# Kernel optimization log

Measured on AMD Instinct MI355X. Metric: run time of the kernel, lower is better.

The kernel has to match this reference:

```python
import jax, jax.numpy as jnp
import numpy as np
import math

B, T, D, H = 2, 2048, 1024, 16
DH = D // H  # 64


def _rope_tables(seq_len, dim, dtype=jnp.float32):
    inv_freq = 1.0 / (10000.0 ** (jnp.arange(0, dim, 2, dtype=jnp.float32) / dim))
    t = jnp.arange(seq_len, dtype=jnp.float32)
    freqs = jnp.outer(t, inv_freq)  # [T, dim/2]
    return jnp.cos(freqs).astype(dtype), jnp.sin(freqs).astype(dtype)


def apply_rotary(x, cos, sin):
    # x: [B,H,T,DH]; cos/sin: [1,1,T,DH/2]
    d = x.shape[-1]
    x1, x2 = x[..., : d // 2], x[..., d // 2 :]
    return jnp.concatenate([x1 * cos - x2 * sin, x2 * cos + x1 * sin], axis=-1)


def setup_inputs() -> dict:
    key = jax.random.key(0)
    k1, k2, k3 = jax.random.split(key, 3)
    x = jax.random.normal(k1, (B, T, D), dtype=jnp.float32)
    Wqkv = jax.random.normal(k2, (D, 3 * D), dtype=jnp.float32) * (1.0 / math.sqrt(D))
    Wout = jax.random.normal(k3, (D, D), dtype=jnp.float32) * (1.0 / math.sqrt(D))
    cos, sin = _rope_tables(T, DH)  # [T, 32]
    mask = jnp.tril(jnp.ones((T, T), dtype=bool))[None, None]  # causal [1,1,T,T]
    return {"x": x, "Wqkv": Wqkv, "Wout": Wout, "cos": cos, "sin": sin, "mask": mask}


def reference(x, Wqkv, Wout, cos, sin, mask):
    Bb, Tt, C = x.shape
    qkv = (x @ Wqkv).reshape(Bb, Tt, 3, H, DH)
    q = jnp.transpose(qkv[:, :, 0], (0, 2, 1, 3))  # [B,H,T,DH]
    k = jnp.transpose(qkv[:, :, 1], (0, 2, 1, 3))
    v = jnp.transpose(qkv[:, :, 2], (0, 2, 1, 3))
    c = cos[None, None]  # [1,1,T,DH/2]
    s = sin[None, None]
    q = apply_rotary(q, c, s)
    k = apply_rotary(k, c, s)
    attn = jnp.einsum("bhqd,bhkd->bhqk", q, k) / math.sqrt(DH)
    attn = jnp.where(mask, attn, jnp.float32(-jnp.inf))
    attn = jax.nn.softmax(attn, axis=-1)  # dropout p=0 (eval)
    out = jnp.einsum("bhqk,bhkd->bhqd", attn, v)
    out = jnp.transpose(out, (0, 2, 1, 3)).reshape(Bb, Tt, C)
    return out @ Wout
```

## Files before the change

### kernel.cpp

```cpp
#include <hip/hip_runtime.h>
#include <hip/hip_bf16.h>

#define B_ 2
#define T_ 2048
#define D_ 1024
#define H_ 16
#define DH_ 64
#define N3_ 3072
#define M_ 4096

typedef __attribute__((ext_vector_type(8))) short short8;
typedef __attribute__((ext_vector_type(4))) float f32x4;
typedef __attribute__((ext_vector_type(4))) unsigned short ushort4v;

__device__ __forceinline__ unsigned short f2bf(float f) {
  return __builtin_bit_cast(unsigned short, __hip_bfloat16(f));
}
__device__ __forceinline__ float bf2f(unsigned short u) {
  union { unsigned u; float f; } v; v.u = ((unsigned)u) << 16;
  return v.f;
}

__device__ __forceinline__ void gload_lds16(const unsigned short* g, unsigned short* l) {
  __builtin_amdgcn_global_load_lds((const __attribute__((address_space(1))) void*)g,
                                   (__attribute__((address_space(3))) void*)l, 16, 0, 0);
}

__global__ __launch_bounds__(256)
void k_cvt(const float* __restrict__ in, unsigned short* __restrict__ out) {
  int i = (blockIdx.x * 256 + threadIdx.x) * 4;
  f32x4 v = *(const f32x4*)&in[i];
  ushort4v o;
  o[0] = f2bf(v[0]); o[1] = f2bf(v[1]); o[2] = f2bf(v[2]); o[3] = f2bf(v[3]);
  *(ushort4v*)&out[i] = o;
}

__global__ __launch_bounds__(256)
void k_transpose(const float* __restrict__ in, unsigned short* __restrict__ out,
                 int R, int C) {
  __shared__ float tile[64][65];
  int c0 = blockIdx.x * 64, r0 = blockIdx.y * 64;
  int tx = threadIdx.x & 63, ty = threadIdx.x >> 6;
#pragma unroll
  for (int i = 0; i < 64; i += 4)
    tile[ty + i][tx] = in[(size_t)(r0 + ty + i) * C + c0 + tx];
  __syncthreads();
#pragma unroll
  for (int i = 0; i < 64; i += 4)
    out[(size_t)(c0 + ty + i) * R + r0 + tx] = f2bf(tile[tx][ty + i]);
}

template <typename OUT_T>
__global__ __launch_bounds__(256)
void k_gemm_bt(const unsigned short* __restrict__ A, const unsigned short* __restrict__ Bt,
               OUT_T* __restrict__ C, int Mx, int Nx, int Kx) {
  __shared__ __align__(16) unsigned short As[128 * 64];
  __shared__ __align__(16) unsigned short Bs[128 * 64];
  const int tid = threadIdx.x;
  const int lane = tid & 63;
  const int l15 = lane & 15, lg = lane >> 4;
  const int l8 = lane >> 3, c8 = lane & 7;
  const int wid = tid >> 6;
  const int wr = wid >> 1, wc = wid & 1;
  const int m0 = blockIdx.y * 128, n0 = blockIdx.x * 128;

  const f32x4 zero4 = {0.f, 0.f, 0.f, 0.f};
  f32x4 acc[4][4];
#pragma unroll
  for (int mi = 0; mi < 4; ++mi)
#pragma unroll
    for (int ni = 0; ni < 4; ++ni) acc[mi][ni] = zero4;

  for (int k0 = 0; k0 < Kx; k0 += 64) {
#pragma unroll
    for (int i = 0; i < 4; ++i)
      gload_lds16(&A[(size_t)(m0 + wid * 32 + i * 8 + l8) * Kx + k0 + c8 * 8],
                  &As[(wid * 32 + i * 8) * 64]);
#pragma unroll
    for (int i = 0; i < 4; ++i)
      gload_lds16(&Bt[(size_t)(n0 + wid * 32 + i * 8 + l8) * Kx + k0 + c8 * 8],
                  &Bs[(wid * 32 + i * 8) * 64]);
    __syncthreads();
#pragma unroll
    for (int kk = 0; kk < 2; ++kk) {
      short8 af[4], bfr[4];
#pragma unroll
      for (int mi = 0; mi < 4; ++mi)
        af[mi] = *(const short8*)&As[(wr * 64 + mi * 16 + l15) * 64 + kk * 32 + lg * 8];
#pragma unroll
      for (int ni = 0; ni < 4; ++ni)
        bfr[ni] = *(const short8*)&Bs[(wc * 64 + ni * 16 + l15) * 64 + kk * 32 + lg * 8];
#pragma unroll
      for (int mi = 0; mi < 4; ++mi)
#pragma unroll
        for (int ni = 0; ni < 4; ++ni)
          acc[mi][ni] = __builtin_amdgcn_mfma_f32_16x16x32_bf16(af[mi], bfr[ni], acc[mi][ni], 0, 0, 0);
    }
    __syncthreads();
  }
#pragma unroll
  for (int mi = 0; mi < 4; ++mi)
#pragma unroll
    for (int ni = 0; ni < 4; ++ni)
#pragma unroll
      for (int j = 0; j < 4; ++j) {
        int row = m0 + wr * 64 + mi * 16 + lg * 4 + j;
        int col = n0 + wc * 64 + ni * 16 + l15;
        float v = acc[mi][ni][j];
        if constexpr (sizeof(OUT_T) == 2) C[(size_t)row * Nx + col] = f2bf(v);
        else                              C[(size_t)row * Nx + col] = v;
      }
}

__global__ __launch_bounds__(256)
void k_gemm_qkv_rope(const unsigned short* __restrict__ A, const unsigned short* __restrict__ Bt,
                     const float* __restrict__ cosT, const float* __restrict__ sinT,
                     unsigned short* __restrict__ Q, unsigned short* __restrict__ K,
                     unsigned short* __restrict__ Vt) {
  __shared__ __align__(16) unsigned short As[128 * 64];
  __shared__ __align__(16) unsigned short Bs[128 * 64];
  const int Kx = D_, Nx = N3_;
  const int tid = threadIdx.x;
  const int lane = tid & 63;
  const int l15 = lane & 15, lg = lane >> 4;
  const int l8 = lane >> 3, c8 = lane & 7;
  const int wid = tid >> 6;
  const int wr = wid >> 1, wc = wid & 1;
  const int m0 = blockIdx.y * 128, n0 = blockIdx.x * 128;

  const f32x4 zero4 = {0.f, 0.f, 0.f, 0.f};
  f32x4 acc[4][4];
#pragma unroll
  for (int mi = 0; mi < 4; ++mi)
#pragma unroll
    for (int ni = 0; ni < 4; ++ni) acc[mi][ni] = zero4;

  for (int k0 = 0; k0 < Kx; k0 += 64) {
#pragma unroll
    for (int i = 0; i < 4; ++i)
      gload_lds16(&A[(size_t)(m0 + wid * 32 + i * 8 + l8) * Kx + k0 + c8 * 8],
                  &As[(wid * 32 + i * 8) * 64]);
#pragma unroll
    for (int i = 0; i < 4; ++i)
      gload_lds16(&Bt[(size_t)(n0 + wid * 32 + i * 8 + l8) * Kx + k0 + c8 * 8],
                  &Bs[(wid * 32 + i * 8) * 64]);
    __syncthreads();
#pragma unroll
    for (int kk = 0; kk < 2; ++kk) {
      short8 af[4], bfr[4];
#pragma unroll
      for (int mi = 0; mi < 4; ++mi)
        af[mi] = *(const short8*)&As[(wr * 64 + mi * 16 + l15) * 64 + kk * 32 + lg * 8];
#pragma unroll
      for (int ni = 0; ni < 4; ++ni)
        bfr[ni] = *(const short8*)&Bs[(wc * 64 + ni * 16 + l15) * 64 + kk * 32 + lg * 8];
#pragma unroll
      for (int mi = 0; mi < 4; ++mi)
#pragma unroll
        for (int ni = 0; ni < 4; ++ni)
          acc[mi][ni] = __builtin_amdgcn_mfma_f32_16x16x32_bf16(af[mi], bfr[ni], acc[mi][ni], 0, 0, 0);
    }
    __syncthreads();
  }

  const int region = n0 >> 10;
  const int h = (((n0 & 1023)) + wc * 64) >> 6;
  if (region < 2) {
    unsigned short* out = (region == 0) ? Q : K;
    const float scale = (region == 0) ? 0.125f : 1.f;
#pragma unroll
    for (int mi = 0; mi < 4; ++mi)
#pragma unroll
      for (int j = 0; j < 4; ++j) {
        int row = m0 + wr * 64 + mi * 16 + lg * 4 + j;
        int b = row >> 11, t = row & (T_ - 1);
        size_t obase = ((size_t)(b * H_ + h) * T_ + t) * DH_;
#pragma unroll
        for (int ni = 0; ni < 2; ++ni) {
          int dh = ni * 16 + l15;
          float cs = cosT[t * 32 + dh], sn = sinT[t * 32 + dh];
          float x1 = acc[mi][ni][j], x2 = acc[mi][ni + 2][j];
          out[obase + dh]      = f2bf((x1 * cs - x2 * sn) * scale);
          out[obase + dh + 32] = f2bf((x2 * cs + x1 * sn) * scale);
        }
      }
  } else {
#pragma unroll
    for (int mi = 0; mi < 4; ++mi) {
      int row0 = m0 + wr * 64 + mi * 16 + lg * 4;
      int b = row0 >> 11, t0 = row0 & (T_ - 1);
#pragma unroll
      for (int ni = 0; ni < 4; ++ni) {
        int col = (n0 - 2048) + wc * 64 + ni * 16 + l15;
        int hv = col >> 6, dh = col & 63;
        ushort4v pk;
#pragma unroll
        for (int j = 0; j < 4; ++j) pk[j] = f2bf(acc[mi][ni][j]);
        *(ushort4v*)&Vt[((size_t)(b * H_ + hv) * DH_ + dh) * T_ + t0] = pk;
      }
    }
  }
}

__global__ __launch_bounds__(256)
void k_attn(const unsigned short* __restrict__ Q, const unsigned short* __restrict__ K,
            const unsigned short* __restrict__ Vt, unsigned short* __restrict__ O) {
  __shared__ __align__(16) unsigned short Ks[2 * 64 * 64];
  __shared__ __align__(16) unsigned short Vs[3 * 64 * 64];
  __shared__ __align__(16) unsigned short Pl[4][16][72];
  const int tid = threadIdx.x;
  const int wid = tid >> 6, lane = tid & 63;
  const int l15 = lane & 15, lg = lane >> 4;
  const int l8 = lane >> 3, c8 = lane & 7;
  const int srcoff = (c8 ^ l8) << 3;
  const int wg = (blockIdx.x & 7) * 128 + (blockIdx.x >> 3);
  const int qb = 31 - (wg & 31);
  const int hb = wg >> 5;
  const int qblk = qb * 64;
  const int q0 = qblk + wid * 16;
  const size_t hbase = (size_t)hb * T_ * DH_;
  const unsigned short* Qh = Q + hbase;
  const unsigned short* Kh = K + hbase;
  const unsigned short* Vh = Vt + hbase;
  unsigned short* Pw = &Pl[wid][0][0];

  short8 bq0 = *(const short8*)&Qh[(q0 + l15) * DH_ + lg * 8];
  short8 bq1 = *(const short8*)&Qh[(q0 + l15) * DH_ + 32 + lg * 8];

  int koffA[4], koffB[4], voff[2][4];
#pragma unroll
  for (int g = 0; g < 4; ++g) {
    int r = g * 16 + l15;
    koffA[g] = r * 64 + (((lg)     ^ (r & 7)) << 3);
    koffB[g] = r * 64 + (((4 + lg) ^ (r & 7)) << 3);
  }
#pragma unroll
  for (int ks = 0; ks < 2; ++ks)
#pragma unroll
    for (int nb = 0; nb < 4; ++nb) {
      int r = nb * 16 + l15;
      voff[ks][nb] = r * 64 + (((ks * 4 + lg) ^ (r & 7)) << 3);
    }

  const f32x4 zero4 = {0.f, 0.f, 0.f, 0.f};
  f32x4 accO[4];
#pragma unroll
  for (int nb = 0; nb < 4; ++nb) accO[nb] = zero4;
  float m_run = -INFINITY, l_run = 0.f;
  const int qg = q0 + l15;
  const int nt = qb + 1;

  auto stage = [&](int t) {
    const int kt = t << 6;
    if (wid < 2) {
      unsigned short* kb = &Ks[(t & 1) * 4096];
      const unsigned short* Kt = Kh + (size_t)kt * DH_;
#pragma unroll
      for (int i = 0; i < 4; ++i)
        gload_lds16(&Kt[(wid * 32 + i * 8 + l8) * DH_ + srcoff],
                    &kb[(wid * 4 + i) * 512]);
    } else {
      unsigned short* vb = &Vs[(t % 3) * 4096];
      const unsigned short* Vg = Vh + kt;
#pragma unroll
      for (int i = 0; i < 4; ++i)
        gload_lds16(&Vg[((wid - 2) * 32 + i * 8 + l8) * T_ + srcoff],
                    &vb[((wid - 2) * 4 + i) * 512]);
    }
  };

  auto QKT = [&](int t, f32x4* cg) {
    const unsigned short* Kb_ = &Ks[(t & 1) * 4096];
#pragma unroll
    for (int g = 0; g < 4; ++g) {
      short8 a0 = *(const short8*)&Kb_[koffA[g]];
      short8 a1 = *(const short8*)&Kb_[koffB[g]];
      cg[g] = __builtin_amdgcn_mfma_f32_16x16x32_bf16(a0, bq0, zero4, 0, 0, 0);
      cg[g] = __builtin_amdgcn_mfma_f32_16x16x32_bf16(a1, bq1, cg[g], 0, 0, 0);
    }
  };

  auto SOFTPV = [&](int t, f32x4* cg) {
    const int kt = t << 6;
    const unsigned short* Vb_ = &Vs[(t % 3) * 4096];
    float s[16];
#pragma unroll
    for (int g = 0; g < 4; ++g)
#pragma unroll
      for (int j = 0; j < 4; ++j) s[g * 4 + j] = cg[g][j];
    if (kt + 63 > q0) {
#pragma unroll
      for (int g = 0; g < 4; ++g) {
        int kb0 = kt + g * 16 + lg * 4;
#pragma unroll
        for (int j = 0; j < 4; ++j)
          if (kb0 + j > qg) s[g * 4 + j] = -INFINITY;
      }
    }
    float t8[8];
#pragma unroll
    for (int j = 0; j < 8; ++j) t8[j] = fmaxf(s[j], s[j + 8]);
    float t4a = fmaxf(t8[0], t8[4]), t4b = fmaxf(t8[1], t8[5]);
    float t4c = fmaxf(t8[2], t8[6]), t4d = fmaxf(t8[3], t8[7]);
    float pm = fmaxf(fmaxf(t4a, t4b), fmaxf(t4c, t4d));
    pm = fmaxf(pm, __shfl_xor(pm, 16));
    pm = fmaxf(pm, __shfl_xor(pm, 32));
    if (!__all(pm <= m_run + 8.f)) {
      float m_new = fmaxf(m_run, pm);
      float alpha = __expf(m_run - m_new);
      float aj[4];
#pragma unroll
      for (int j = 0; j < 4; ++j) aj[j] = __shfl(alpha, lg * 4 + j);
#pragma unroll
      for (int nb = 0; nb < 4; ++nb)
#pragma unroll
        for (int j = 0; j < 4; ++j) accO[nb][j] *= aj[j];
      l_run *= alpha;
      m_run = m_new;
    }
    float p[16];
#pragma unroll
    for (int j = 0; j < 16; ++j) p[j] = __expf(s[j] - m_run);
    float u8[8];
#pragma unroll
    for (int j = 0; j < 8; ++j) u8[j] = p[j] + p[j + 8];
    float u4a = u8[0] + u8[4], u4b = u8[1] + u8[5];
    float u4c = u8[2] + u8[6], u4d = u8[3] + u8[7];
    float psum = (u4a + u4b) + (u4c + u4d);
    psum += __shfl_xor(psum, 16);
    psum += __shfl_xor(psum, 32);
    l_run += psum;
#pragma unroll
    for (int g = 0; g < 4; ++g) {
      ushort4v pk;
#pragma unroll
      for (int j = 0; j < 4; ++j) pk[j] = f2bf(p[g * 4 + j]);
      *(ushort4v*)&Pw[l15 * 72 + g * 16 + lg * 4] = pk;
    }
#pragma unroll
    for (int ks = 0; ks < 2; ++ks) {
      short8 pa = *(const short8*)&Pw[l15 * 72 + ks * 32 + lg * 8];
#pragma unroll
      for (int nb = 0; nb < 4; ++nb) {
        short8 vb = *(const short8*)&Vb_[voff[ks][nb]];
        accO[nb] = __builtin_amdgcn_mfma_f32_16x16x32_bf16(pa, vb, accO[nb], 0, 0, 0);
      }
    }
  };

  f32x4 cgA[4], cgB[4];
  stage(0);
  for (int t = 0; t < nt; t += 2) {
    __syncthreads();
    if (t + 1 < nt) stage(t + 1);
    QKT(t, cgA);
    if (t > 0) SOFTPV(t - 1, cgB);
    __syncthreads();
    if (t + 2 < nt) stage(t + 2);
    if (t + 1 < nt) QKT(t + 1, cgB);
    SOFTPV(t, cgA);
  }
  if ((nt & 1) == 0) SOFTPV(nt - 1, cgB);

  float lj[4];
#pragma unroll
  for (int j = 0; j < 4; ++j) lj[j] = 1.f / __shfl(l_run, lg * 4 + j);
  int b = hb >> 4, h = hb & 15;
#pragma unroll
  for (int nb = 0; nb < 4; ++nb)
#pragma unroll
    for (int j = 0; j < 4; ++j) {
      int t = q0 + lg * 4 + j;
      O[(size_t)(b * T_ + t) * D_ + h * DH_ + nb * 16 + l15] = f2bf(accO[nb][j] * lj[j]);
    }
}

extern "C" void kernel_launch(void* const* d_in, const int* in_sizes, int n_in,
                              void* d_out, int out_size, void* d_ws, size_t ws_size,
                              hipStream_t stream) {
  const float* x    = (const float*)d_in[0];
  const float* Wqkv = (const float*)d_in[1];
  const float* Wout = (const float*)d_in[2];
  const float* cosT = (const float*)d_in[3];
  const float* sinT = (const float*)d_in[4];
  float* out = (float*)d_out;
  char* ws = (char*)d_ws;
  unsigned short* Xb     = (unsigned short*)(ws);
  unsigned short* Wqkv_t = (unsigned short*)(ws + 8388608);
  unsigned short* Wout_t = (unsigned short*)(ws + 14680064);
  unsigned short* Ob     = (unsigned short*)(ws + 16777216);
  unsigned short* Qb     = (unsigned short*)(ws + 41943040);
  unsigned short* Kb     = (unsigned short*)(ws + 50331648);
  unsigned short* Vt     = (unsigned short*)(ws + 58720256);

  k_cvt<<<4096, 256, 0, stream>>>(x, Xb);
  k_transpose<<<dim3(48, 16), 256, 0, stream>>>(Wqkv, Wqkv_t, 1024, 3072);
  k_transpose<<<dim3(16, 16), 256, 0, stream>>>(Wout, Wout_t, 1024, 1024);
  k_gemm_qkv_rope<<<dim3(24, 32), 256, 0, stream>>>(Xb, Wqkv_t, cosT, sinT, Qb, Kb, Vt);
  k_attn<<<1024, 256, 0, stream>>>(Qb, Kb, Vt, Ob);
  k_gemm_bt<float><<<dim3(8, 32), 256, 0, stream>>>(Ob, Wout_t, out, 4096, 1024, 1024);
}
```

Measured before the change: 149.7 us.

## Double-buffer GEMM LDS tiles with XOR swizzle and single barrier per step

Both the projection GEMM and the fused QKV+RoPE GEMM now stage 32-wide K slices into two LDS buffers, loading the next slice while computing on the current one with one barrier per iteration. Global-to-LDS source addresses and fragment reads use an XOR swizzle to avoid LDS bank conflicts on the 16-byte fragment loads. This aims to hide global load latency and cut bank conflicts, at the cost of twice as many loop iterations and more index arithmetic.

Result: faster. 135.1 us (median of 2 runs) (-9.7%).

```diff
diff --git a/kernel.cpp b/kernel.cpp
--- a/kernel.cpp
+++ b/kernel.cpp
@@ -50,16 +50,53 @@
     out[(size_t)(c0 + ty + i) * R + r0 + tx] = f2bf(tile[tx][ty + i]);
 }
 
+#define GEMM_DBUF_LOOP(A_, Bt_, Kx_)                                               \
+  const int l4 = lane >> 2, c4 = lane & 3;                                         \
+  const int srcswz = ((c4 ^ (l4 & 3) ^ ((l4 >> 2) & 3)) << 3);                     \
+  const int fswz = (((l15 & 3) ^ ((l15 >> 2) & 3)) << 3);                          \
+  auto stage = [&](int buf, int k0) {                                              \
+    _Pragma("unroll")                                                              \
+    for (int i = 0; i < 2; ++i)                                                    \
+      gload_lds16(&A_[(size_t)(m0 + wid * 32 + i * 16 + l4) * Kx_ + k0 + srcswz],  \
+                  &As[buf * 4096 + (wid * 32 + i * 16) * 32]);                     \
+    _Pragma("unroll")                                                              \
+    for (int i = 0; i < 2; ++i)                                                    \
+      gload_lds16(&Bt_[(size_t)(n0 + wid * 32 + i * 16 + l4) * Kx_ + k0 + srcswz], \
+                  &Bs[buf * 4096 + (wid * 32 + i * 16) * 32]);                     \
+  };                                                                               \
+  const int KI = (Kx_) >> 5;                                                       \
+  stage(0, 0);                                                                     \
+  for (int it = 0; it < KI; ++it) {                                                \
+    __syncthreads();                                                               \
+    if (it + 1 < KI) stage((it + 1) & 1, (it + 1) << 5);                           \
+    const unsigned short* As_ = &As[(it & 1) * 4096];                              \
+    const unsigned short* Bs_ = &Bs[(it & 1) * 4096];                              \
+    short8 af[4], bfr[4];                                                          \
+    _Pragma("unroll")                                                              \
+    for (int mi = 0; mi < 4; ++mi)                                                 \
+      af[mi] = *(const short8*)&As_[(wr * 64 + mi * 16 + l15) * 32 +               \
+                                    ((lg << 3) ^ fswz)];                           \
+    _Pragma("unroll")                                                              \
+    for (int ni = 0; ni < 4; ++ni)                                                 \
+      bfr[ni] = *(const short8*)&Bs_[(wc * 64 + ni * 16 + l15) * 32 +              \
+                                     ((lg << 3) ^ fswz)];                          \
+    _Pragma("unroll")                                                              \
+    for (int mi = 0; mi < 4; ++mi)                                                 \
+      _Pragma("unroll")                                                            \
+      for (int ni = 0; ni < 4; ++ni)                                               \
+        acc[mi][ni] = __builtin_amdgcn_mfma_f32_16x16x32_bf16(af[mi], bfr[ni],     \
+                                                              acc[mi][ni], 0, 0, 0); \
+  }
+
 template <typename OUT_T>
 __global__ __launch_bounds__(256)
 void k_gemm_bt(const unsigned short* __restrict__ A, const unsigned short* __restrict__ Bt,
                OUT_T* __restrict__ C, int Mx, int Nx, int Kx) {
-  __shared__ __align__(16) unsigned short As[128 * 64];
-  __shared__ __align__(16) unsigned short Bs[128 * 64];
+  __shared__ __align__(16) unsigned short As[2 * 128 * 32];
+  __shared__ __align__(16) unsigned short Bs[2 * 128 * 32];
   const int tid = threadIdx.x;
   const int lane = tid & 63;
   const int l15 = lane & 15, lg = lane >> 4;
-  const int l8 = lane >> 3, c8 = lane & 7;
   const int wid = tid >> 6;
   const int wr = wid >> 1, wc = wid & 1;
   const int m0 = blockIdx.y * 128, n0 = blockIdx.x * 128;
@@ -71,33 +108,8 @@
 #pragma unroll
     for (int ni = 0; ni < 4; ++ni) acc[mi][ni] = zero4;
 
-  for (int k0 = 0; k0 < Kx; k0 += 64) {
-#pragma unroll
-    for (int i = 0; i < 4; ++i)
-      gload_lds16(&A[(size_t)(m0 + wid * 32 + i * 8 + l8) * Kx + k0 + c8 * 8],
-                  &As[(wid * 32 + i * 8) * 64]);
-#pragma unroll
-    for (int i = 0; i < 4; ++i)
-      gload_lds16(&Bt[(size_t)(n0 + wid * 32 + i * 8 + l8) * Kx + k0 + c8 * 8],
-                  &Bs[(wid * 32 + i * 8) * 64]);
-    __syncthreads();
-#pragma unroll
-    for (int kk = 0; kk < 2; ++kk) {
-      short8 af[4], bfr[4];
-#pragma unroll
-      for (int mi = 0; mi < 4; ++mi)
-        af[mi] = *(const short8*)&As[(wr * 64 + mi * 16 + l15) * 64 + kk * 32 + lg * 8];
-#pragma unroll
-      for (int ni = 0; ni < 4; ++ni)
-        bfr[ni] = *(const short8*)&Bs[(wc * 64 + ni * 16 + l15) * 64 + kk * 32 + lg * 8];
-#pragma unroll
-      for (int mi = 0; mi < 4; ++mi)
-#pragma unroll
-        for (int ni = 0; ni < 4; ++ni)
-          acc[mi][ni] = __builtin_amdgcn_mfma_f32_16x16x32_bf16(af[mi], bfr[ni], acc[mi][ni], 0, 0, 0);
-    }
-    __syncthreads();
-  }
+  GEMM_DBUF_LOOP(A, Bt, Kx)
+
 #pragma unroll
   for (int mi = 0; mi < 4; ++mi)
 #pragma unroll
@@ -117,13 +129,11 @@
                      const float* __restrict__ cosT, const float* __restrict__ sinT,
                      unsigned short* __restrict__ Q, unsigned short* __restrict__ K,
                      unsigned short* __restrict__ Vt) {
-  __shared__ __align__(16) unsigned short As[128 * 64];
-  __shared__ __align__(16) unsigned short Bs[128 * 64];
-  const int Kx = D_, Nx = N3_;
+  __shared__ __align__(16) unsigned short As[2 * 128 * 32];
+  __shared__ __align__(16) unsigned short Bs[2 * 128 * 32];
   const int tid = threadIdx.x;
   const int lane = tid & 63;
   const int l15 = lane & 15, lg = lane >> 4;
-  const int l8 = lane >> 3, c8 = lane & 7;
   const int wid = tid >> 6;
   const int wr = wid >> 1, wc = wid & 1;
   const int m0 = blockIdx.y * 128, n0 = blockIdx.x * 128;
@@ -135,33 +145,7 @@
 #pragma unroll
     for (int ni = 0; ni < 4; ++ni) acc[mi][ni] = zero4;
 
-  for (int k0 = 0; k0 < Kx; k0 += 64) {
-#pragma unroll
-    for (int i = 0; i < 4; ++i)
-      gload_lds16(&A[(size_t)(m0 + wid * 32 + i * 8 + l8) * Kx + k0 + c8 * 8],
-                  &As[(wid * 32 + i * 8) * 64]);
-#pragma unroll
-    for (int i = 0; i < 4; ++i)
-      gload_lds16(&Bt[(size_t)(n0 + wid * 32 + i * 8 + l8) * Kx + k0 + c8 * 8],
-                  &Bs[(wid * 32 + i * 8) * 64]);
-    __syncthreads();
-#pragma unroll
-    for (int kk = 0; kk < 2; ++kk) {
-      short8 af[4], bfr[4];
-#pragma unroll
-      for (int mi = 0; mi < 4; ++mi)
-        af[mi] = *(const short8*)&As[(wr * 64 + mi * 16 + l15) * 64 + kk * 32 + lg * 8];
-#pragma unroll
-      for (int ni = 0; ni < 4; ++ni)
-        bfr[ni] = *(const short8*)&Bs[(wc * 64 + ni * 16 + l15) * 64 + kk * 32 + lg * 8];
-#pragma unroll
-      for (int mi = 0; mi < 4; ++mi)
-#pragma unroll
-        for (int ni = 0; ni < 4; ++ni)
-          acc[mi][ni] = __builtin_amdgcn_mfma_f32_16x16x32_bf16(af[mi], bfr[ni], acc[mi][ni], 0, 0, 0);
-    }
-    __syncthreads();
-  }
+  GEMM_DBUF_LOOP(A, Bt, D_)
 
   const int region = n0 >> 10;
   const int h = (((n0 & 1023)) + wc * 64) >> 6;
```
